# Kernel optimization log

Hardware: AMD Instinct MI355X
Metric: run time of the kernel (lower is better)

## Reference

```python
import jax, jax.numpy as jnp
import numpy as np

D_MODEL = 1024
HEADS = 16
HEAD_DIM = D_MODEL // HEADS


def setup_inputs() -> dict:
    key = jax.random.key(0)
    ks = jax.random.split(key, 9)
    s = 1.0 / np.sqrt(D_MODEL)
    inp = {
        "inputs": jax.random.normal(ks[0], (4, 2048, D_MODEL), dtype=jnp.float32),
        "Wq": jax.random.normal(ks[1], (D_MODEL, D_MODEL), dtype=jnp.float32) * s,
        "bq": jnp.zeros((D_MODEL,), dtype=jnp.float32),
        "Wk": jax.random.normal(ks[2], (D_MODEL, D_MODEL), dtype=jnp.float32) * s,
        "bk": jnp.zeros((D_MODEL,), dtype=jnp.float32),
        "Wv": jax.random.normal(ks[3], (D_MODEL, D_MODEL), dtype=jnp.float32) * s,
        "bv": jnp.zeros((D_MODEL,), dtype=jnp.float32),
        "Wo": jax.random.normal(ks[4], (D_MODEL, D_MODEL), dtype=jnp.float32) * s,
        "bo": jnp.zeros((D_MODEL,), dtype=jnp.float32),
    }
    return inp


def reference(inputs, Wq, bq, Wk, bk, Wv, bv, Wo, bo):
    bs, seq, _ = inputs.shape
    # projections -> [b, h, s, d]
    def split_heads(x):
        return x.reshape(bs, seq, HEADS, HEAD_DIM).transpose(0, 2, 1, 3)
    q = split_heads(inputs @ Wq + bq)
    k = split_heads(inputs @ Wk + bk)
    v = split_heads(inputs @ Wv + bv)
    # NOTE: original code divides by (head_dim ** 1 / 2) == head_dim/2, not sqrt(head_dim)
    scale = HEAD_DIM / 2.0
    scores = jnp.einsum("bhqd,bhkd->bhqk", q, k) / scale
    attn = jax.nn.softmax(scores, axis=-1)
    out = jnp.einsum("bhqk,bhkd->bhqd", attn, v)
    out = out.transpose(0, 2, 1, 3).reshape(bs, seq, HEADS * HEAD_DIM)
    return out @ Wo + bo
```

## Files before the change

kernel.cpp:

```cpp
#include <hip/hip_runtime.h>
#include <stdint.h>

typedef __attribute__((ext_vector_type(8))) short bf16x8;
typedef __attribute__((ext_vector_type(4))) float f32x4;
typedef __attribute__((address_space(1))) void as1_void;
typedef __attribute__((address_space(3))) void as3_void;

#define D_MODEL 1024
#define SEQ     2048
#define BATCH   4
#define HEADS   16
#define HDIM    64

#define QSCALE 0.045084220029218407f

__device__ __forceinline__ ushort f2bf(float f) {
  union { float f; unsigned u; } v; v.f = f;
  unsigned u = v.u + 0x7fffu + ((v.u >> 16) & 1u);
  return (ushort)(u >> 16);
}

__device__ __forceinline__ void gload_lds16(const void* g, void* l) {
  __builtin_amdgcn_global_load_lds((as1_void*)(uintptr_t)g, (as3_void*)l, 16, 0, 0);
}

__device__ __forceinline__ bf16x8 pack8(float a0, float a1, float a2, float a3,
                                        float a4, float a5, float a6, float a7) {
  union { uint u[4]; bf16x8 v; } x;
  x.u[0] = __builtin_amdgcn_perm(__float_as_uint(a1), __float_as_uint(a0), 0x07060302);
  x.u[1] = __builtin_amdgcn_perm(__float_as_uint(a3), __float_as_uint(a2), 0x07060302);
  x.u[2] = __builtin_amdgcn_perm(__float_as_uint(a5), __float_as_uint(a4), 0x07060302);
  x.u[3] = __builtin_amdgcn_perm(__float_as_uint(a7), __float_as_uint(a6), 0x07060302);
  return x.v;
}

__global__ void prep_kernel(const float* __restrict__ X,
                            const float* w0, const float* w1, const float* w2, const float* w3,
                            const float* __restrict__ bq, const float* __restrict__ bk,
                            const float* __restrict__ bv,
                            ushort* __restrict__ Xb, ushort* __restrict__ WT,
                            float* __restrict__ bcat) {
  __shared__ float tile[32][33];
  const int bx = blockIdx.x, t = threadIdx.x;
  if (bx < 8192) {
    int i = bx * 256 + t;
    float4 f = reinterpret_cast<const float4*>(X)[i];
    ushort4 o;
    o.x = f2bf(f.x); o.y = f2bf(f.y); o.z = f2bf(f.z); o.w = f2bf(f.w);
    reinterpret_cast<ushort4*>(Xb)[i] = o;
  } else if (bx < 12288) {
    int tz = bx - 8192;
    int z = tz >> 10;
    int xy = tz & 1023;
    int bxt = xy & 31, byt = xy >> 5;
    const float* w = (z == 0) ? w0 : (z == 1) ? w1 : (z == 2) ? w2 : w3;
    const float sc = (z == 0) ? QSCALE : 1.0f;
    ushort* o = WT + (size_t)z * D_MODEL * D_MODEL;
    int tx = t & 31, ty = t >> 5;
    int x = bxt * 32 + tx;
    int y0 = byt * 32;
    #pragma unroll
    for (int i = ty; i < 32; i += 8)
      tile[i][tx] = w[(size_t)(y0 + i) * D_MODEL + x];
    __syncthreads();
    #pragma unroll
    for (int i = ty; i < 32; i += 8)
      o[(size_t)(bxt * 32 + i) * D_MODEL + y0 + tx] = f2bf(tile[tx][i] * sc);
  } else {
    int i = (bx - 12288) * 256 + t;
    bcat[i] = (i < 1024) ? bq[i] * QSCALE : (i < 2048) ? bk[i - 1024] : bv[i - 2048];
  }
}

__global__ __launch_bounds__(256) void gemm_qkv(const ushort* __restrict__ A, const ushort* __restrict__ BT,
                                                const float* __restrict__ bias,
                                                ushort* __restrict__ QK, ushort* __restrict__ Vt) {
  __shared__ __align__(16) ushort As[128 * 32];
  __shared__ __align__(16) ushort Bs[128 * 32];
  const int K = D_MODEL;
  const int tid  = threadIdx.x;
  const int w    = tid >> 6;
  const int lane = tid & 63;
  const int lo   = lane & 15, quad = lane >> 4;
  const int m0 = blockIdx.y * 128, n0 = blockIdx.x * 128;
  const int ra = lane >> 2;
  const int ca = (lane & 3) * 8;
  const int wm = (w & 1) * 64, wn = (w >> 1) * 64;

  f32x4 acc[4][4];
  #pragma unroll
  for (int i = 0; i < 4; ++i)
    #pragma unroll
    for (int j = 0; j < 4; ++j) acc[i][j] = {0.f, 0.f, 0.f, 0.f};

  for (int k0 = 0; k0 < K; k0 += 32) {
    #pragma unroll
    for (int i = 0; i < 2; ++i) {
      const int j = w * 2 + i;
      gload_lds16(A  + (size_t)(m0 + j * 16 + ra) * K + k0 + ca, &As[j * 512]);
      gload_lds16(BT + (size_t)(n0 + j * 16 + ra) * K + k0 + ca, &Bs[j * 512]);
    }
    __syncthreads();
    bf16x8 af[4], bfv[4];
    #pragma unroll
    for (int mi = 0; mi < 4; ++mi) af[mi]  = *(const bf16x8*)&As[(wm + mi * 16 + lo) * 32 + quad * 8];
    #pragma unroll
    for (int ni = 0; ni < 4; ++ni) bfv[ni] = *(const bf16x8*)&Bs[(wn + ni * 16 + lo) * 32 + quad * 8];
    #pragma unroll
    for (int mi = 0; mi < 4; ++mi)
      #pragma unroll
      for (int ni = 0; ni < 4; ++ni)
        acc[mi][ni] = __builtin_amdgcn_mfma_f32_16x16x32_bf16(af[mi], bfv[ni], acc[mi][ni], 0, 0, 0);
    __syncthreads();
  }

  if (blockIdx.x < 16) {
    #pragma unroll
    for (int ni = 0; ni < 4; ++ni) {
      const int col = n0 + wn + ni * 16 + lo;
      const float bv = bias[col];
      #pragma unroll
      for (int mi = 0; mi < 4; ++mi) {
        #pragma unroll
        for (int r = 0; r < 4; ++r) {
          const int row = m0 + wm + mi * 16 + quad * 4 + r;
          QK[(size_t)row * 2048 + col] = f2bf(acc[mi][ni][r] + bv);
        }
      }
    }
  } else {
    #pragma unroll
    for (int ni = 0; ni < 4; ++ni) {
      const int col  = n0 + wn + ni * 16 + lo;
      const int vcol = col - 2048;
      const int hh = vcol >> 6, d = vcol & 63;
      const float bv = bias[col];
      #pragma unroll
      for (int mi = 0; mi < 4; ++mi) {
        const int base = m0 + wm + mi * 16;
        const int brow = base + quad * 4;
        const int bidx = brow >> 11;
        const int srow = brow & 2047;
        const int ck   = srow >> 6;
        const int c0   = (base & 32) + (quad << 3) + ((base >> 2) & 4);
        ushort e0 = f2bf(acc[mi][ni][0] + bv);
        ushort e1 = f2bf(acc[mi][ni][1] + bv);
        ushort e2 = f2bf(acc[mi][ni][2] + bv);
        ushort e3 = f2bf(acc[mi][ni][3] + bv);
        uint2 pk;
        pk.x = (uint)e0 | ((uint)e1 << 16);
        pk.y = (uint)e2 | ((uint)e3 << 16);
        *(uint2*)&Vt[(size_t)((bidx * HEADS + hh) * HDIM + d) * SEQ + ck * 64 + c0] = pk;
      }
    }
  }
}

__global__ __launch_bounds__(256) void gemm_bt_f32(const ushort* __restrict__ A, const ushort* __restrict__ BT,
                                                   const float* __restrict__ bias, float* __restrict__ C,
                                                   int M, int N, int K) {
  __shared__ __align__(16) ushort As[128 * 32];
  __shared__ __align__(16) ushort Bs[128 * 32];
  const int tid  = threadIdx.x;
  const int w    = tid >> 6;
  const int lane = tid & 63;
  const int lo   = lane & 15, quad = lane >> 4;
  const int m0 = blockIdx.y * 128, n0 = blockIdx.x * 128;
  const int ra = lane >> 2;
  const int ca = (lane & 3) * 8;
  const int wm = (w & 1) * 64, wn = (w >> 1) * 64;

  f32x4 acc[4][4];
  #pragma unroll
  for (int i = 0; i < 4; ++i)
    #pragma unroll
    for (int j = 0; j < 4; ++j) acc[i][j] = {0.f, 0.f, 0.f, 0.f};

  for (int k0 = 0; k0 < K; k0 += 32) {
    #pragma unroll
    for (int i = 0; i < 2; ++i) {
      const int j = w * 2 + i;
      gload_lds16(A  + (size_t)(m0 + j * 16 + ra) * K + k0 + ca, &As[j * 512]);
      gload_lds16(BT + (size_t)(n0 + j * 16 + ra) * K + k0 + ca, &Bs[j * 512]);
    }
    __syncthreads();
    bf16x8 af[4], bfv[4];
    #pragma unroll
    for (int mi = 0; mi < 4; ++mi) af[mi]  = *(const bf16x8*)&As[(wm + mi * 16 + lo) * 32 + quad * 8];
    #pragma unroll
    for (int ni = 0; ni < 4; ++ni) bfv[ni] = *(const bf16x8*)&Bs[(wn + ni * 16 + lo) * 32 + quad * 8];
    #pragma unroll
    for (int mi = 0; mi < 4; ++mi)
      #pragma unroll
      for (int ni = 0; ni < 4; ++ni)
        acc[mi][ni] = __builtin_amdgcn_mfma_f32_16x16x32_bf16(af[mi], bfv[ni], acc[mi][ni], 0, 0, 0);
    __syncthreads();
  }

  #pragma unroll
  for (int ni = 0; ni < 4; ++ni) {
    const int col = n0 + wn + ni * 16 + lo;
    const float bv = bias[col];
    #pragma unroll
    for (int mi = 0; mi < 4; ++mi) {
      #pragma unroll
      for (int r = 0; r < 4; ++r) {
        const int row = m0 + wm + mi * 16 + quad * 4 + r;
        C[(size_t)row * N + col] = acc[mi][ni][r] + bv;
      }
    }
  }
}

__global__ __launch_bounds__(256, 2) void attn_kernel(const ushort* __restrict__ QK,
                                                      const ushort* __restrict__ Vt,
                                                      ushort* __restrict__ Og) {
  __shared__ __align__(16) ushort Ks[64 * 64];
  __shared__ __align__(16) ushort Vs[64 * 64];

  const int tid  = threadIdx.x;
  const int w    = tid >> 6, lane = tid & 63;
  const int lo   = lane & 15, quad = lane >> 4;
  const int h = blockIdx.y, b = blockIdx.z;
  const int qbase = blockIdx.x * 256 + w * 64;
  const int swz = lo & 7;

  bf16x8 qf[4][2];
  #pragma unroll
  for (int qg = 0; qg < 4; ++qg) {
    const ushort* qp = QK + (size_t)(b * SEQ + qbase + qg * 16 + lo) * 2048 + h * HDIM;
    qf[qg][0] = *(const bf16x8*)(qp + quad * 8);
    qf[qg][1] = *(const bf16x8*)(qp + 32 + quad * 8);
  }

  f32x4 acc[4][4];
  #pragma unroll
  for (int qg = 0; qg < 4; ++qg)
    #pragma unroll
    for (int t = 0; t < 4; ++t) acc[qg][t] = {0.f, 0.f, 0.f, 0.f};
  float lsum[4] = {0.f, 0.f, 0.f, 0.f};

  for (int ck = 0; ck < SEQ / 64; ++ck) {
    __syncthreads();
    #pragma unroll
    for (int i = 0; i < 2; ++i) {
      const int c16 = (w * 2 + i) * 64 + lane;
      const int r = c16 >> 3, ps = c16 & 7;
      const int gs = ps ^ (r & 7);
      gload_lds16(QK + (size_t)(b * SEQ + ck * 64 + r) * 2048 + 1024 + h * HDIM + gs * 8,
                  &Ks[(w * 2 + i) * 512]);
      gload_lds16(Vt + (size_t)((b * HEADS + h) * HDIM + r) * SEQ + ck * 64 + gs * 8,
                  &Vs[(w * 2 + i) * 512]);
    }
    __syncthreads();

    bf16x8 kf[4][2];
    #pragma unroll
    for (int sub = 0; sub < 4; ++sub) {
      const ushort* kr = &Ks[(sub * 16 + lo) * 64];
      kf[sub][0] = *(const bf16x8*)(kr + ((quad ^ swz) * 8));
      kf[sub][1] = *(const bf16x8*)(kr + (((4 + quad) ^ swz) * 8));
    }

    bf16x8 af[4][2];
    #pragma unroll
    for (int qg = 0; qg < 4; ++qg) {
      f32x4 s[4];
      #pragma unroll
      for (int sub = 0; sub < 4; ++sub) s[sub] = {0.f, 0.f, 0.f, 0.f};
      #pragma unroll
      for (int sub = 0; sub < 4; ++sub) {
        s[sub] = __builtin_amdgcn_mfma_f32_16x16x32_bf16(kf[sub][0], qf[qg][0], s[sub], 0, 0, 0);
        s[sub] = __builtin_amdgcn_mfma_f32_16x16x32_bf16(kf[sub][1], qf[qg][1], s[sub], 0, 0, 0);
      }
      float p[4][4];
      #pragma unroll
      for (int sub = 0; sub < 4; ++sub)
        #pragma unroll
        for (int r = 0; r < 4; ++r) p[sub][r] = __builtin_amdgcn_exp2f(s[sub][r]);
      float t0 = 0.f;
      #pragma unroll
      for (int sub = 0; sub < 4; ++sub)
        t0 += (p[sub][0] + p[sub][1]) + (p[sub][2] + p[sub][3]);
      lsum[qg] += t0;
      af[qg][0] = pack8(p[0][0], p[0][1], p[0][2], p[0][3], p[1][0], p[1][1], p[1][2], p[1][3]);
      af[qg][1] = pack8(p[2][0], p[2][1], p[2][2], p[2][3], p[3][0], p[3][1], p[3][2], p[3][3]);
    }

    #pragma unroll
    for (int t = 0; t < 4; ++t) {
      const ushort* vr = &Vs[(t * 16 + lo) * 64];
      #pragma unroll
      for (int hh = 0; hh < 2; ++hh) {
        bf16x8 vf = *(const bf16x8*)(vr + (((hh * 4 + quad) ^ swz) * 8));
        #pragma unroll
        for (int qg = 0; qg < 4; ++qg)
          acc[qg][t] = __builtin_amdgcn_mfma_f32_16x16x32_bf16(af[qg][hh], vf, acc[qg][t], 0, 0, 0);
      }
    }
  }

  #pragma unroll
  for (int qg = 0; qg < 4; ++qg) {
    float v = lsum[qg];
    v += __shfl_xor(v, 16);
    v += __shfl_xor(v, 32);
    float linv[4];
    #pragma unroll
    for (int r = 0; r < 4; ++r) linv[r] = 1.0f / __shfl(v, quad * 4 + r);
    #pragma unroll
    for (int t = 0; t < 4; ++t)
      #pragma unroll
      for (int r = 0; r < 4; ++r)
        Og[(size_t)(b * SEQ + qbase + qg * 16 + quad * 4 + r) * D_MODEL + h * HDIM + t * 16 + lo] =
            f2bf(acc[qg][t][r] * linv[r]);
  }
}

extern "C" void kernel_launch(void* const* d_in, const int* in_sizes, int n_in,
                              void* d_out, int out_size, void* d_ws, size_t ws_size,
                              hipStream_t stream) {
  const float* X  = (const float*)d_in[0];
  const float* Wq = (const float*)d_in[1];
  const float* bq = (const float*)d_in[2];
  const float* Wk = (const float*)d_in[3];
  const float* bk = (const float*)d_in[4];
  const float* Wv = (const float*)d_in[5];
  const float* bv = (const float*)d_in[6];
  const float* Wo = (const float*)d_in[7];
  const float* bo = (const float*)d_in[8];
  float* out = (float*)d_out;
  char* ws = (char*)d_ws;

  ushort* Xb  = (ushort*)(ws);
  ushort* WT  = (ushort*)(ws + 16777216);
  ushort* QKb = (ushort*)(ws + 25165824);
  ushort* Vtb = (ushort*)(ws + 58720256);
  ushort* Ob  = (ushort*)(ws + 75497472);
  float*  bcat = (float*)(ws + 75497472);
  const int WSTRIDE = D_MODEL * D_MODEL;

  prep_kernel<<<12300, 256, 0, stream>>>(X, Wq, Wk, Wv, Wo, bq, bk, bv, Xb, WT, bcat);

  gemm_qkv<<<dim3(24, 64), 256, 0, stream>>>(Xb, WT, bcat, QKb, Vtb);

  attn_kernel<<<dim3(SEQ / 256, HEADS, BATCH), 256, 0, stream>>>(QKb, Vtb, Ob);

  gemm_bt_f32<<<dim3(8, 64), 256, 0, stream>>>(Ob, WT + 3 * WSTRIDE, bo, out,
                                               BATCH * SEQ, D_MODEL, D_MODEL);
}
```

Measured before the change: 272.1 us.

## Double-buffer LDS tiles in QKV GEMM, output GEMM and attention kernels

Adds two LDS buffers to the QKV projection GEMM, the output projection GEMM and the attention K/V loop. The next K-slice or key/value chunk is prefetched with global_load_lds into the alternate buffer while MFMAs run on the current one, and each iteration now needs only one barrier instead of two. The aim is to hide global-memory latency behind matrix math and cut barrier stalls. The cost is twice the LDS per block, which could lower occupancy, and the design relies on the barrier draining the outstanding DMA loads. The output GEMM also hardcodes its M/N/K sizes.

```diff
diff --git a/kernel.cpp b/kernel.cpp
--- a/kernel.cpp
+++ b/kernel.cpp
@@ -75,8 +75,8 @@
 __global__ __launch_bounds__(256) void gemm_qkv(const ushort* __restrict__ A, const ushort* __restrict__ BT,
                                                 const float* __restrict__ bias,
                                                 ushort* __restrict__ QK, ushort* __restrict__ Vt) {
-  __shared__ __align__(16) ushort As[128 * 32];
-  __shared__ __align__(16) ushort Bs[128 * 32];
+  __shared__ __align__(16) ushort As[2][4096];
+  __shared__ __align__(16) ushort Bs[2][4096];
   const int K = D_MODEL;
   const int tid  = threadIdx.x;
   const int w    = tid >> 6;
@@ -93,25 +93,35 @@
     #pragma unroll
     for (int j = 0; j < 4; ++j) acc[i][j] = {0.f, 0.f, 0.f, 0.f};
 
-  for (int k0 = 0; k0 < K; k0 += 32) {
-    #pragma unroll
-    for (int i = 0; i < 2; ++i) {
-      const int j = w * 2 + i;
-      gload_lds16(A  + (size_t)(m0 + j * 16 + ra) * K + k0 + ca, &As[j * 512]);
-      gload_lds16(BT + (size_t)(n0 + j * 16 + ra) * K + k0 + ca, &Bs[j * 512]);
-    }
+  #pragma unroll
+  for (int i = 0; i < 2; ++i) {
+    const int j = w * 2 + i;
+    gload_lds16(A  + (size_t)(m0 + j * 16 + ra) * K + ca, &As[0][j * 512]);
+    gload_lds16(BT + (size_t)(n0 + j * 16 + ra) * K + ca, &Bs[0][j * 512]);
+  }
+
+  for (int it = 0; it < 32; ++it) {
+    const int buf = it & 1;
     __syncthreads();
+    if (it < 31) {
+      const int kk = (it + 1) * 32;
+      #pragma unroll
+      for (int i = 0; i < 2; ++i) {
+        const int j = w * 2 + i;
+        gload_lds16(A  + (size_t)(m0 + j * 16 + ra) * K + kk + ca, &As[buf ^ 1][j * 512]);
+        gload_lds16(BT + (size_t)(n0 + j * 16 + ra) * K + kk + ca, &Bs[buf ^ 1][j * 512]);
+      }
+    }
     bf16x8 af[4], bfv[4];
     #pragma unroll
-    for (int mi = 0; mi < 4; ++mi) af[mi]  = *(const bf16x8*)&As[(wm + mi * 16 + lo) * 32 + quad * 8];
-    #pragma unroll
-    for (int ni = 0; ni < 4; ++ni) bfv[ni] = *(const bf16x8*)&Bs[(wn + ni * 16 + lo) * 32 + quad * 8];
+    for (int mi = 0; mi < 4; ++mi) af[mi]  = *(const bf16x8*)&As[buf][(wm + mi * 16 + lo) * 32 + quad * 8];
+    #pragma unroll
+    for (int ni = 0; ni < 4; ++ni) bfv[ni] = *(const bf16x8*)&Bs[buf][(wn + ni * 16 + lo) * 32 + quad * 8];
     #pragma unroll
     for (int mi = 0; mi < 4; ++mi)
       #pragma unroll
       for (int ni = 0; ni < 4; ++ni)
         acc[mi][ni] = __builtin_amdgcn_mfma_f32_16x16x32_bf16(af[mi], bfv[ni], acc[mi][ni], 0, 0, 0);
-    __syncthreads();
   }
 
   if (blockIdx.x < 16) {
@@ -157,10 +167,10 @@
 }
 
 __global__ __launch_bounds__(256) void gemm_bt_f32(const ushort* __restrict__ A, const ushort* __restrict__ BT,
-                                                   const float* __restrict__ bias, float* __restrict__ C,
-                                                   int M, int N, int K) {
-  __shared__ __align__(16) ushort As[128 * 32];
-  __shared__ __align__(16) ushort Bs[128 * 32];
+                                                   const float* __restrict__ bias, float* __restrict__ C) {
+  __shared__ __align__(16) ushort As[2][4096];
+  __shared__ __align__(16) ushort Bs[2][4096];
+  const int K = D_MODEL, N = D_MODEL;
   const int tid  = threadIdx.x;
   const int w    = tid >> 6;
   const int lane = tid & 63;
@@ -176,25 +186,35 @@
     #pragma unroll
     for (int j = 0; j < 4; ++j) acc[i][j] = {0.f, 0.f, 0.f, 0.f};
 
-  for (int k0 = 0; k0 < K; k0 += 32) {
-    #pragma unroll
-    for (int i = 0; i < 2; ++i) {
-      const int j = w * 2 + i;
-      gload_lds16(A  + (size_t)(m0 + j * 16 + ra) * K + k0 + ca, &As[j * 512]);
-      gload_lds16(BT + (size_t)(n0 + j * 16 + ra) * K + k0 + ca, &Bs[j * 512]);
-    }
+  #pragma unroll
+  for (int i = 0; i < 2; ++i) {
+    const int j = w * 2 + i;
+    gload_lds16(A  + (size_t)(m0 + j * 16 + ra) * K + ca, &As[0][j * 512]);
+    gload_lds16(BT + (size_t)(n0 + j * 16 + ra) * K + ca, &Bs[0][j * 512]);
+  }
+
+  for (int it = 0; it < 32; ++it) {
+    const int buf = it & 1;
     __syncthreads();
+    if (it < 31) {
+      const int kk = (it + 1) * 32;
+      #pragma unroll
+      for (int i = 0; i < 2; ++i) {
+        const int j = w * 2 + i;
+        gload_lds16(A  + (size_t)(m0 + j * 16 + ra) * K + kk + ca, &As[buf ^ 1][j * 512]);
+        gload_lds16(BT + (size_t)(n0 + j * 16 + ra) * K + kk + ca, &Bs[buf ^ 1][j * 512]);
+      }
+    }
     bf16x8 af[4], bfv[4];
     #pragma unroll
-    for (int mi = 0; mi < 4; ++mi) af[mi]  = *(const bf16x8*)&As[(wm + mi * 16 + lo) * 32 + quad * 8];
-    #pragma unroll
-    for (int ni = 0; ni < 4; ++ni) bfv[ni] = *(const bf16x8*)&Bs[(wn + ni * 16 + lo) * 32 + quad * 8];
+    for (int mi = 0; mi < 4; ++mi) af[mi]  = *(const bf16x8*)&As[buf][(wm + mi * 16 + lo) * 32 + quad * 8];
+    #pragma unroll
+    for (int ni = 0; ni < 4; ++ni) bfv[ni] = *(const bf16x8*)&Bs[buf][(wn + ni * 16 + lo) * 32 + quad * 8];
     #pragma unroll
     for (int mi = 0; mi < 4; ++mi)
       #pragma unroll
       for (int ni = 0; ni < 4; ++ni)
         acc[mi][ni] = __builtin_amdgcn_mfma_f32_16x16x32_bf16(af[mi], bfv[ni], acc[mi][ni], 0, 0, 0);
-    __syncthreads();
   }
 
   #pragma unroll
@@ -215,8 +235,8 @@
 __global__ __launch_bounds__(256, 2) void attn_kernel(const ushort* __restrict__ QK,
                                                       const ushort* __restrict__ Vt,
                                                       ushort* __restrict__ Og) {
-  __shared__ __align__(16) ushort Ks[64 * 64];
-  __shared__ __align__(16) ushort Vs[64 * 64];
+  __shared__ __align__(16) ushort Ks[2][4096];
+  __shared__ __align__(16) ushort Vs[2][4096];
 
   const int tid  = threadIdx.x;
   const int w    = tid >> 6, lane = tid & 63;
@@ -225,6 +245,19 @@
   const int qbase = blockIdx.x * 256 + w * 64;
   const int swz = lo & 7;
 
+  const ushort* ksrc[2];
+  const ushort* vsrc[2];
+  int slotr[2];
+  #pragma unroll
+  for (int i = 0; i < 2; ++i) {
+    const int c16 = (w * 2 + i) * 64 + lane;
+    const int r = c16 >> 3, ps = c16 & 7;
+    const int gs = ps ^ (r & 7);
+    slotr[i] = (w * 2 + i) * 512;
+    ksrc[i] = QK + (size_t)(b * SEQ + r) * 2048 + 1024 + h * HDIM + gs * 8;
+    vsrc[i] = Vt + (size_t)((b * HEADS + h) * HDIM + r) * SEQ + gs * 8;
+  }
+
   bf16x8 qf[4][2];
   #pragma unroll
   for (int qg = 0; qg < 4; ++qg) {
@@ -240,24 +273,27 @@
     for (int t = 0; t < 4; ++t) acc[qg][t] = {0.f, 0.f, 0.f, 0.f};
   float lsum[4] = {0.f, 0.f, 0.f, 0.f};
 
+  #pragma unroll
+  for (int i = 0; i < 2; ++i) {
+    gload_lds16(ksrc[i], &Ks[0][slotr[i]]);
+    gload_lds16(vsrc[i], &Vs[0][slotr[i]]);
+  }
+
   for (int ck = 0; ck < SEQ / 64; ++ck) {
+    const int buf = ck & 1;
     __syncthreads();
-    #pragma unroll
-    for (int i = 0; i < 2; ++i) {
-      const int c16 = (w * 2 + i) * 64 + lane;
-      const int r = c16 >> 3, ps = c16 & 7;
-      const int gs = ps ^ (r & 7);
-      gload_lds16(QK + (size_t)(b * SEQ + ck * 64 + r) * 2048 + 1024 + h * HDIM + gs * 8,
-                  &Ks[(w * 2 + i) * 512]);
-      gload_lds16(Vt + (size_t)((b * HEADS + h) * HDIM + r) * SEQ + ck * 64 + gs * 8,
-                  &Vs[(w * 2 + i) * 512]);
-    }
-    __syncthreads();
+    if (ck + 1 < SEQ / 64) {
+      #pragma unroll
+      for (int i = 0; i < 2; ++i) {
+        gload_lds16(ksrc[i] + (size_t)(ck + 1) * 64 * 2048, &Ks[buf ^ 1][slotr[i]]);
+        gload_lds16(vsrc[i] + (size_t)(ck + 1) * 64,        &Vs[buf ^ 1][slotr[i]]);
+      }
+    }
 
     bf16x8 kf[4][2];
     #pragma unroll
     for (int sub = 0; sub < 4; ++sub) {
-      const ushort* kr = &Ks[(sub * 16 + lo) * 64];
+      const ushort* kr = &Ks[buf][(sub * 16 + lo) * 64];
       kf[sub][0] = *(const bf16x8*)(kr + ((quad ^ swz) * 8));
       kf[sub][1] = *(const bf16x8*)(kr + (((4 + quad) ^ swz) * 8));
     }
@@ -289,7 +325,7 @@
 
     #pragma unroll
     for (int t = 0; t < 4; ++t) {
-      const ushort* vr = &Vs[(t * 16 + lo) * 64];
+      const ushort* vr = &Vs[buf][(t * 16 + lo) * 64];
       #pragma unroll
       for (int hh = 0; hh < 2; ++hh) {
         bf16x8 vf = *(const bf16x8*)(vr + (((hh * 4 + quad) ^ swz) * 8));
@@ -346,6 +382,5 @@
 
   attn_kernel<<<dim3(SEQ / 256, HEADS, BATCH), 256, 0, stream>>>(QKb, Vtb, Ob);
 
-  gemm_bt_f32<<<dim3(8, 64), 256, 0, stream>>>(Ob, WT + 3 * WSTRIDE, bo, out,
-                                               BATCH * SEQ, D_MODEL, D_MODEL);
-}
+  gemm_bt_f32<<<dim3(8, 64), 256, 0, stream>>>(Ob, WT + 3 * WSTRIDE, bo, out);
+}
```

Result: slower. 290.5 us (+6.8%).

## Store Q/K head-major and stream K/V from global into registers in attention

Applied to the files above, without the earlier changes.

The QKV GEMM now writes Q and K in a per-(batch,head) contiguous [seq, 64] layout instead of an interleaved [row, 2048] buffer. The attention kernel drops its LDS staging and barriers, loading K and V fragments straight from global memory into registers and double-buffering the next K chunk while computing the current one. The grid is reordered so blocks of the same batch-head are adjacent, which is meant to help L2 reuse of K/V. The trade-off is that each wave now issues its own global loads of K/V with no sharing through LDS, and the extra register buffers may raise pressure (the launch-bounds occupancy hint was also removed).

```diff
diff --git a/kernel.cpp b/kernel.cpp
--- a/kernel.cpp
+++ b/kernel.cpp
@@ -74,7 +74,8 @@
 
 __global__ __launch_bounds__(256) void gemm_qkv(const ushort* __restrict__ A, const ushort* __restrict__ BT,
                                                 const float* __restrict__ bias,
-                                                ushort* __restrict__ QK, ushort* __restrict__ Vt) {
+                                                ushort* __restrict__ Qh, ushort* __restrict__ Kh,
+                                                ushort* __restrict__ Vt) {
   __shared__ __align__(16) ushort As[128 * 32];
   __shared__ __align__(16) ushort Bs[128 * 32];
   const int K = D_MODEL;
@@ -119,12 +120,16 @@
     for (int ni = 0; ni < 4; ++ni) {
       const int col = n0 + wn + ni * 16 + lo;
       const float bv = bias[col];
+      const int head = (col >> 6) & 15;
+      const int d = col & 63;
+      ushort* dst = (col < 1024) ? Qh : Kh;
       #pragma unroll
       for (int mi = 0; mi < 4; ++mi) {
         #pragma unroll
         for (int r = 0; r < 4; ++r) {
           const int row = m0 + wm + mi * 16 + quad * 4 + r;
-          QK[(size_t)row * 2048 + col] = f2bf(acc[mi][ni][r] + bv);
+          const int bidx = row >> 11, srow = row & 2047;
+          dst[(size_t)((bidx * HEADS + head) * SEQ + srow) * HDIM + d] = f2bf(acc[mi][ni][r] + bv);
         }
       }
     }
@@ -157,10 +162,10 @@
 }
 
 __global__ __launch_bounds__(256) void gemm_bt_f32(const ushort* __restrict__ A, const ushort* __restrict__ BT,
-                                                   const float* __restrict__ bias, float* __restrict__ C,
-                                                   int M, int N, int K) {
+                                                   const float* __restrict__ bias, float* __restrict__ C) {
   __shared__ __align__(16) ushort As[128 * 32];
   __shared__ __align__(16) ushort Bs[128 * 32];
+  const int K = D_MODEL, N = D_MODEL;
   const int tid  = threadIdx.x;
   const int w    = tid >> 6;
   const int lane = tid & 63;
@@ -212,25 +217,27 @@
   }
 }
 
-__global__ __launch_bounds__(256, 2) void attn_kernel(const ushort* __restrict__ QK,
-                                                      const ushort* __restrict__ Vt,
-                                                      ushort* __restrict__ Og) {
-  __shared__ __align__(16) ushort Ks[64 * 64];
-  __shared__ __align__(16) ushort Vs[64 * 64];
-
+__global__ __launch_bounds__(256) void attn_kernel(const ushort* __restrict__ Qh,
+                                                   const ushort* __restrict__ Kh,
+                                                   const ushort* __restrict__ Vt,
+                                                   ushort* __restrict__ Og) {
   const int tid  = threadIdx.x;
   const int w    = tid >> 6, lane = tid & 63;
   const int lo   = lane & 15, quad = lane >> 4;
-  const int h = blockIdx.y, b = blockIdx.z;
-  const int qbase = blockIdx.x * 256 + w * 64;
-  const int swz = lo & 7;
+  const int bh = blockIdx.x;
+  const int b = bh >> 4, h = bh & 15;
+  const int qbase = blockIdx.y * 256 + w * 64;
+
+  const ushort* Qbh = Qh + (size_t)bh * SEQ * HDIM;
+  const ushort* Kbh = Kh + (size_t)bh * SEQ * HDIM;
+  const ushort* Vbh = Vt + (size_t)bh * HDIM * SEQ;
 
   bf16x8 qf[4][2];
   #pragma unroll
   for (int qg = 0; qg < 4; ++qg) {
-    const ushort* qp = QK + (size_t)(b * SEQ + qbase + qg * 16 + lo) * 2048 + h * HDIM;
-    qf[qg][0] = *(const bf16x8*)(qp + quad * 8);
-    qf[qg][1] = *(const bf16x8*)(qp + 32 + quad * 8);
+    const ushort* qp = Qbh + (size_t)(qbase + qg * 16 + lo) * HDIM + quad * 8;
+    qf[qg][0] = *(const bf16x8*)(qp);
+    qf[qg][1] = *(const bf16x8*)(qp + 32);
   }
 
   f32x4 acc[4][4];
@@ -240,27 +247,26 @@
     for (int t = 0; t < 4; ++t) acc[qg][t] = {0.f, 0.f, 0.f, 0.f};
   float lsum[4] = {0.f, 0.f, 0.f, 0.f};
 
-  for (int ck = 0; ck < SEQ / 64; ++ck) {
-    __syncthreads();
-    #pragma unroll
-    for (int i = 0; i < 2; ++i) {
-      const int c16 = (w * 2 + i) * 64 + lane;
-      const int r = c16 >> 3, ps = c16 & 7;
-      const int gs = ps ^ (r & 7);
-      gload_lds16(QK + (size_t)(b * SEQ + ck * 64 + r) * 2048 + 1024 + h * HDIM + gs * 8,
-                  &Ks[(w * 2 + i) * 512]);
-      gload_lds16(Vt + (size_t)((b * HEADS + h) * HDIM + r) * SEQ + ck * 64 + gs * 8,
-                  &Vs[(w * 2 + i) * 512]);
-    }
-    __syncthreads();
-
-    bf16x8 kf[4][2];
+  bf16x8 kfa[4][2], kfb[4][2];
+  auto load_kf = [&](int ck, bf16x8 kf[4][2]) {
     #pragma unroll
     for (int sub = 0; sub < 4; ++sub) {
-      const ushort* kr = &Ks[(sub * 16 + lo) * 64];
-      kf[sub][0] = *(const bf16x8*)(kr + ((quad ^ swz) * 8));
-      kf[sub][1] = *(const bf16x8*)(kr + (((4 + quad) ^ swz) * 8));
-    }
+      const ushort* kr = Kbh + (size_t)(ck * 64 + sub * 16 + lo) * HDIM + quad * 8;
+      kf[sub][0] = *(const bf16x8*)(kr);
+      kf[sub][1] = *(const bf16x8*)(kr + 32);
+    }
+  };
+
+  auto do_chunk = [&](int ck, const bf16x8 kf[4][2], bf16x8 kfn[4][2]) {
+    bf16x8 vf[4][2];
+    #pragma unroll
+    for (int t = 0; t < 4; ++t) {
+      const ushort* vr = Vbh + (size_t)(t * 16 + lo) * SEQ + ck * 64 + quad * 8;
+      vf[t][0] = *(const bf16x8*)(vr);
+      vf[t][1] = *(const bf16x8*)(vr + 32);
+    }
+    const int ckn = (ck + 1 < SEQ / 64) ? ck + 1 : ck;
+    load_kf(ckn, kfn);
 
     bf16x8 af[4][2];
     #pragma unroll
@@ -288,16 +294,18 @@
     }
 
     #pragma unroll
-    for (int t = 0; t < 4; ++t) {
-      const ushort* vr = &Vs[(t * 16 + lo) * 64];
-      #pragma unroll
-      for (int hh = 0; hh < 2; ++hh) {
-        bf16x8 vf = *(const bf16x8*)(vr + (((hh * 4 + quad) ^ swz) * 8));
+    for (int t = 0; t < 4; ++t)
+      #pragma unroll
+      for (int hh = 0; hh < 2; ++hh)
         #pragma unroll
         for (int qg = 0; qg < 4; ++qg)
-          acc[qg][t] = __builtin_amdgcn_mfma_f32_16x16x32_bf16(af[qg][hh], vf, acc[qg][t], 0, 0, 0);
-      }
-    }
+          acc[qg][t] = __builtin_amdgcn_mfma_f32_16x16x32_bf16(af[qg][hh], vf[t][hh], acc[qg][t], 0, 0, 0);
+  };
+
+  load_kf(0, kfa);
+  for (int ck = 0; ck < SEQ / 64; ck += 2) {
+    do_chunk(ck,     kfa, kfb);
+    do_chunk(ck + 1, kfb, kfa);
   }
 
   #pragma unroll
@@ -334,7 +342,8 @@
 
   ushort* Xb  = (ushort*)(ws);
   ushort* WT  = (ushort*)(ws + 16777216);
-  ushort* QKb = (ushort*)(ws + 25165824);
+  ushort* Qhb = (ushort*)(ws + 25165824);
+  ushort* Khb = (ushort*)(ws + 41943040);
   ushort* Vtb = (ushort*)(ws + 58720256);
   ushort* Ob  = (ushort*)(ws + 75497472);
   float*  bcat = (float*)(ws + 75497472);
@@ -342,10 +351,9 @@
 
   prep_kernel<<<12300, 256, 0, stream>>>(X, Wq, Wk, Wv, Wo, bq, bk, bv, Xb, WT, bcat);
 
-  gemm_qkv<<<dim3(24, 64), 256, 0, stream>>>(Xb, WT, bcat, QKb, Vtb);
-
-  attn_kernel<<<dim3(SEQ / 256, HEADS, BATCH), 256, 0, stream>>>(QKb, Vtb, Ob);
-
-  gemm_bt_f32<<<dim3(8, 64), 256, 0, stream>>>(Ob, WT + 3 * WSTRIDE, bo, out,
-                                               BATCH * SEQ, D_MODEL, D_MODEL);
-}
+  gemm_qkv<<<dim3(24, 64), 256, 0, stream>>>(Xb, WT, bcat, Qhb, Khb, Vtb);
+
+  attn_kernel<<<dim3(BATCH * HEADS, SEQ / 256), 256, 0, stream>>>(Qhb, Khb, Vtb, Ob);
+
+  gemm_bt_f32<<<dim3(8, 64), 256, 0, stream>>>(Ob, WT + 3 * WSTRIDE, bo, out);
+}
```

Measured after the change: 330.8 us. +21.6%, slower.
